# Kernel tuning notes

Hardware: AMD Instinct MI355X
Metric: run time of the kernel (lower is better)

The kernel has to match this reference:

```python
import jax, jax.numpy as jnp
import numpy as np

B, DIM, W0, H0 = 4, 256, 128, 128
HEADS, HEAD_DIM = 8, 32
FOLD, PROP = 2, 4
EPS_GN = 1e-5


def _l2norm(x):
    n = jnp.linalg.norm(x, axis=-1, keepdims=True)
    return x / jnp.maximum(n, 1e-12)  # matches F.normalize eps


def _fold(t, f):
    # (b, c, f*w, f*h) -> (b*f*f, c, w, h), matching einops '(b f1 f2)' ordering
    b, c, W, H = t.shape
    w, h = W // f, H // f
    return t.reshape(b, c, f, w, f, h).transpose(0, 2, 4, 1, 3, 5).reshape(b * f * f, c, w, h)


def _unfold(t, f, b0):
    bf, c, w, h = t.shape
    return t.reshape(b0, f, f, c, w, h).transpose(0, 3, 1, 4, 2, 5).reshape(b0, c, f * w, f * h)


def _pool(t, p):
    # AdaptiveAvgPool2d((p, p)) for divisible sizes
    b, c, w, h = t.shape
    return t.reshape(b, c, p, w // p, p, h // p).mean(axis=(3, 5))


def setup_inputs() -> dict:
    key = jax.random.key(0)
    ks = jax.random.split(key, 6)
    D = HEADS * HEAD_DIM
    return {
        "x": jax.random.normal(ks[0], (B, DIM, W0, H0), jnp.float32),
        "xyz": jax.random.normal(ks[1], (B, 3, W0, H0), jnp.float32),
        "Wv": jax.random.normal(ks[2], (D, DIM, 7, 7), jnp.float32) * 0.02,
        "bv": jnp.zeros((D,), jnp.float32),
        "Wproj": jax.random.normal(ks[3], (DIM, D), jnp.float32) * 0.02,
        "bproj": jnp.zeros((DIM,), jnp.float32),
        "gn_w": jnp.ones((D,), jnp.float32),
        "gn_b": jnp.zeros((D,), jnp.float32),
        "sim_alpha": jnp.ones((1,), jnp.float32),
        "sim_beta": jnp.zeros((1,), jnp.float32),
    }


def reference(x, xyz, Wv, bv, Wproj, bproj, gn_w, gn_b, sim_alpha, sim_beta):
    # value = self.v(x): 7x7 conv, padding 3
    value = jax.lax.conv_general_dilated(
        x, Wv, (1, 1), ((3, 3), (3, 3)),
        dimension_numbers=("NCHW", "OIHW", "NCHW")) + bv[None, :, None, None]
    b0 = x.shape[0]
    # heads split: 'b (e c) w h -> (b e) c w h'
    xh = x.reshape(b0 * HEADS, HEAD_DIM, W0, H0)
    vh = value.reshape(b0 * HEADS, HEAD_DIM, W0, H0)
    xf = _fold(xh, FOLD)
    vf = _fold(vh, FOLD)
    xyzf = _fold(xyz, FOLD)
    bb, c, w, h = xf.shape
    M = PROP * PROP
    N = w * h
    centers = _pool(xf, PROP)                                   # (bb, c, p, p)
    xyz_c = _pool(xyzf, PROP)
    value_centers = _pool(vf, PROP).reshape(bb, c, M).transpose(0, 2, 1)  # (bb, M, c)
    cen = centers.reshape(bb, c, M).transpose(0, 2, 1)          # (bb, M, c)
    xpts = xf.reshape(bb, c, N).transpose(0, 2, 1)              # (bb, N, c)
    vpts = vf.reshape(bb, c, N).transpose(0, 2, 1)              # (bb, N, c)
    sim = jax.nn.sigmoid(sim_beta + sim_alpha *
                         jnp.einsum('bmc,bnc->bmn', _l2norm(cen), _l2norm(xpts)))
    bg = xyzf.shape[0]
    xyz_pts = xyzf.reshape(bg, 3, N).transpose(0, 2, 1)
    xyz_cc = xyz_c.reshape(bg, 3, M).transpose(0, 2, 1)
    sim_geo = jax.nn.sigmoid(sim_beta + sim_alpha *
                             jnp.einsum('bmc,bnc->bmn', _l2norm(xyz_cc), _l2norm(xyz_pts)))
    sim_geo = jnp.tile(sim_geo, (sim.shape[0] // sim_geo.shape[0], 1, 1))  # torch .repeat
    sim = sim * sim_geo ** 2
    # faithful mask math: scatter_(1, argmax, 1.0) into an all-ones tensor leaves it all-ones,
    # so dense_mask == 1 and split_mask == 0 exactly as in the source.
    dense_mask = jnp.ones_like(sim)
    split_mask = 1.0 - dense_mask
    denss_sim = sim * dense_mask
    split_sim = sim * split_mask
    split_out = (jnp.einsum('bmn,bnc->bmc', split_sim, vpts) + value_centers) \
                / (split_sim.sum(-1, keepdims=True) + 1.0)
    denss_out = (jnp.einsum('bmn,bnc->bmc', denss_sim, xpts) + cen) \
                / (denss_sim.sum(-1, keepdims=True) + 1.0)
    denss_pts = jnp.einsum('bmc,bmn->bnc', denss_out, denss_sim)  # (bb, N, c)
    split_pts = jnp.einsum('bmc,bmn->bnc', split_out, split_sim)
    out = (denss_pts + split_pts).transpose(0, 2, 1).reshape(bb, c, w, h)
    out = _unfold(out, FOLD, b0 * HEADS)
    out = out.reshape(b0, HEADS * HEAD_DIM, W0, H0)
    # GroupNorm with 1 group: normalize over (C, H, W) per sample
    mu = out.mean(axis=(1, 2, 3), keepdims=True)
    var = ((out - mu) ** 2).mean(axis=(1, 2, 3), keepdims=True)
    out = (out - mu) / jnp.sqrt(var + EPS_GN)
    out = out * gn_w[None, :, None, None] + gn_b[None, :, None, None]
    # proj 1x1 conv + silu
    out = jnp.einsum('bchw,oc->bohw', out, Wproj) + bproj[None, :, None, None]
    return jax.nn.silu(out)
```

## Files before the change

### kernel.cpp

```cpp
#include <hip/hip_runtime.h>
#include <stdint.h>


typedef __attribute__((ext_vector_type(8))) short short8;
typedef __attribute__((ext_vector_type(4))) float floatx4;
typedef __fp16 fp16x2 __attribute__((ext_vector_type(2)));

#define SIMS_DW 260

__device__ float g_sbp[2048*2];
__device__ float g_alpha[1024];
__device__ float g_bias[1024];
__device__ __attribute__((aligned(16))) _Float16 g_Wa[4*256*256];
__device__ float g_cenraw[128*16*32];
__device__ float g_cenhat[128*16*32];
__device__ float g_gcenhat[16*16*4];
__device__ __attribute__((aligned(16))) _Float16 g_sim[(size_t)128*4096*16];
__device__ float g_dnum[128*16*16*32];
__device__ float g_rsum[128*16*16];
__device__ unsigned g_dnh2[128*256];
__device__ __attribute__((aligned(16))) _Float16 g_preout[(size_t)128*4096*32];

static __device__ __forceinline__ fp16x2 as_h2(unsigned u) { return __builtin_bit_cast(fp16x2, u); }
static __device__ __forceinline__ unsigned pk(float a, float b) {
  return __builtin_bit_cast(unsigned, __builtin_amdgcn_cvt_pkrtz(a, b));
}
#if __has_builtin(__builtin_amdgcn_fdot2)
static __device__ __forceinline__ float fdot2(fp16x2 a, fp16x2 b, float c) {
  return __builtin_amdgcn_fdot2(a, b, c, false);
}
#else
static __device__ __forceinline__ float fdot2(fp16x2 a, fp16x2 b, float c) {
  return c + (float)a[0]*(float)b[0] + (float)a[1]*(float)b[1];
}
#endif
static __device__ __forceinline__ float sum16(const float* p) {
  const float4* q = (const float4*)p;
  float4 a = q[0], b = q[1], c = q[2], d = q[3];
  return (a.x+a.y+a.z+a.w) + (b.x+b.y+b.z+b.w) + (c.x+c.y+c.z+c.w) + (d.x+d.y+d.z+d.w);
}
static __device__ __forceinline__ float sigm(float z) {
  return __builtin_amdgcn_rcpf(1.f + __expf(-z));
}

__global__ __launch_bounds__(64) void k0_geo(const float* __restrict__ xyz) {
  __shared__ float gc[64];
  const int gti = blockIdx.x;
  const int bg = gti >> 2, f1 = (gti >> 1) & 1, f2 = gti & 1;
  const int t = threadIdx.x;
  if (t < 48) {
    const int m = t / 3, ch = t - 3*(t/3);
    const int pi = m >> 2, pj = m & 3;
    const float* p = xyz + (size_t)(bg*3+ch)*16384 + (f1*64 + pi*16)*128 + f2*64 + pj*16;
    float s = 0.f;
    #pragma unroll
    for (int r = 0; r < 16; ++r) s += sum16(p + r*128);
    gc[m*4+ch] = s * (1.f/256.f);
  }
  __syncthreads();
  if (t < 16) {
    float g0 = gc[t*4], g1 = gc[t*4+1], g2 = gc[t*4+2];
    float inv = 1.f / fmaxf(sqrtf(g0*g0+g1*g1+g2*g2), 1e-12f);
    float* o = g_gcenhat + gti*64 + t*4;
    o[0] = g0*inv; o[1] = g1*inv; o[2] = g2*inv; o[3] = 0.f;
  }
}

__global__ __launch_bounds__(128) void k1a_cen(const float* __restrict__ x) {
  __shared__ float cenL[128];
  __shared__ float invL[4];
  const int blk = blockIdx.x;
  const int bb = blk >> 2, pi = blk & 3;
  const int b = bb >> 5, e = (bb >> 2) & 7, f1 = (bb >> 1) & 1, f2 = bb & 1;
  const int tid = threadIdx.x;
  const int c = tid >> 2, pj = tid & 3;
  const int m = pi*4 + pj;
  const float* p = x + ((size_t)(b*256 + e*32 + c)*128 + f1*64 + pi*16)*128 + f2*64 + pj*16;
  float s = 0.f;
  #pragma unroll
  for (int r = 0; r < 16; ++r) s += sum16(p + r*128);
  const float raw = s * (1.f/256.f);
  cenL[pj*32 + c] = raw;
  g_cenraw[(bb*16 + m)*32 + c] = raw;
  __syncthreads();
  if (tid < 4) {
    float ss = 0.f;
    #pragma unroll
    for (int cc = 0; cc < 32; ++cc) { float v = cenL[tid*32+cc]; ss += v*v; }
    invL[tid] = 1.f / fmaxf(sqrtf(ss), 1e-12f);
  }
  __syncthreads();
  g_cenhat[(bb*16 + m)*32 + c] = raw * invL[pj];
}

__global__ __launch_bounds__(256, 4) void k1b_sim(const float* __restrict__ x,
                                                  const float* __restrict__ xyz,
                                                  const float* __restrict__ salpha,
                                                  const float* __restrict__ sbeta) {
  __shared__ float simS[16*SIMS_DW];
  __shared__ unsigned chP[256];
  __shared__ float gcenL[64];
  __shared__ float rsW[64];
  const int blk = blockIdx.x;
  const int bb = blk >> 4, ck = blk & 15;
  const int b = bb >> 5, e = (bb >> 2) & 7, f1 = (bb >> 1) & 1, f2 = bb & 1;
  const int gti = ((e & 3) << 2) | (f1 << 1) | f2;
  const int tid = threadIdx.x, lane = tid & 63, wave = tid >> 6;
  const float alpha = salpha[0], beta = sbeta[0];
  const float* xt = x + (((size_t)(b*256 + e*32))*128 + f1*64)*128 + f2*64;

  {
    const float2 cp = *(const float2*)(g_cenhat + bb*512 + tid*2);
    chP[tid] = pk(cp.x, cp.y);
  }
  if (tid < 64) gcenL[tid] = g_gcenhat[gti*64 + tid];
  __syncthreads();

  const int ng = ck*256 + tid;
  const int wi = ng >> 6, hi = ng & 63;
  const int addr = wi*128 + hi;
  float xn[32]; float ss = 0.f;
  #pragma unroll
  for (int c = 0; c < 32; ++c) { float v = xt[(size_t)c*16384 + addr]; xn[c] = v; ss += v*v; }
  unsigned xp[16];
  #pragma unroll
  for (int p = 0; p < 16; ++p) xp[p] = pk(xn[2*p], xn[2*p+1]);
  const float invn = __builtin_amdgcn_rcpf(fmaxf(sqrtf(ss), 1e-12f));
  float g0, g1, g2;
  {
    const float* gp = xyz + (size_t)((e & 3)*3)*16384 + (f1*64 + wi)*128 + f2*64 + hi;
    g0 = gp[0]; g1 = gp[16384]; g2 = gp[32768];
    float invg = __builtin_amdgcn_rcpf(fmaxf(sqrtf(g0*g0+g1*g1+g2*g2), 1e-12f));
    g0 *= invg; g1 *= invg; g2 *= invg;
  }
  float svf[16];
  #pragma unroll
  for (int m = 0; m < 16; ++m) {
    float d = 0.f;
    #pragma unroll
    for (int p = 0; p < 16; ++p) d = fdot2(as_h2(chP[m*16+p]), as_h2(xp[p]), d);
    d *= invn;
    const float* gh = gcenL + m*4;
    const float dg = gh[0]*g0 + gh[1]*g1 + gh[2]*g2;
    const float s  = sigm(beta + alpha*d);
    const float gg = sigm(beta + alpha*dg);
    const float sv = s*gg*gg;
    svf[m] = sv;
    simS[m*SIMS_DW + tid] = sv;
  }
  {
    uint4 o0, o1;
    o0.x = pk(svf[0],svf[1]);   o0.y = pk(svf[2],svf[3]);
    o0.z = pk(svf[4],svf[5]);   o0.w = pk(svf[6],svf[7]);
    o1.x = pk(svf[8],svf[9]);   o1.y = pk(svf[10],svf[11]);
    o1.z = pk(svf[12],svf[13]); o1.w = pk(svf[14],svf[15]);
    _Float16* gp = g_sim + ((size_t)bb*4096 + ng)*16;
    *(uint4*)gp = o0;
    *(uint4*)(gp + 8) = o1;
  }
  #pragma unroll
  for (int m = 0; m < 16; ++m) {
    float v = svf[m];
    #pragma unroll
    for (int off = 1; off < 64; off <<= 1) v += __shfl_xor(v, off, 64);
    if (lane == 0) rsW[wave*16 + m] = v;
  }
  __syncthreads();
  if (tid < 16) g_rsum[(bb*16 + ck)*16 + tid] = rsW[tid] + rsW[16+tid] + rsW[32+tid] + rsW[48+tid];

  #pragma unroll
  for (int t2 = 0; t2 < 2; ++t2) {
    const int task = tid + t2*256;
    const int m = task & 15, c = task >> 4;
    const float* sp = simS + m*SIMS_DW;
    const float* px = xt + (size_t)c*16384 + ck*512;
    float acc = 0.f;
    #pragma unroll 2
    for (int j = 0; j < 32; ++j) {
      const int a0 = (j >> 3)*128 + (j & 7)*8;
      const float4 xa = *(const float4*)(px + a0);
      const float4 xb = *(const float4*)(px + a0 + 4);
      const float4 sa = *(const float4*)(sp + j*8);
      const float4 sb = *(const float4*)(sp + j*8 + 4);
      acc += sa.x*xa.x + sa.y*xa.y + sa.z*xa.z + sa.w*xa.w
           + sb.x*xb.x + sb.y*xb.y + sb.z*xb.z + sb.w*xb.w;
    }
    g_dnum[(((size_t)bb*16 + ck)*16 + m)*32 + c] = acc;
  }
}

__global__ __launch_bounds__(512) void k1c_red() {
  __shared__ float denssL[512];
  __shared__ float rsL[16];
  const int bb = blockIdx.x, tid = threadIdx.x;
  if (tid < 16) {
    float r = 1.f;
    #pragma unroll
    for (int k = 0; k < 16; ++k) r += g_rsum[(bb*16 + k)*16 + tid];
    rsL[tid] = r;
  }
  float a = g_cenraw[bb*512 + tid];
  #pragma unroll
  for (int k = 0; k < 16; ++k) a += g_dnum[(size_t)bb*8192 + k*512 + tid];
  __syncthreads();
  denssL[tid] = a / rsL[tid >> 5];
  __syncthreads();
  if (tid < 256) {
    const int c = tid >> 3, mp = tid & 7;
    g_dnh2[bb*256 + c*8 + mp] = pk(denssL[(2*mp)*32 + c], denssL[(2*mp+1)*32 + c]);
  }
}

__global__ __launch_bounds__(256, 4) void k1d_out() {
  __shared__ unsigned dl[256];
  __shared__ float sred[8];
  const int blk = blockIdx.x;
  const int bb = blk >> 4, ck = blk & 15;
  const int tid = threadIdx.x, lane = tid & 63, wave = tid >> 6;
  dl[tid] = g_dnh2[bb*256 + tid];
  __syncthreads();
  const int ng = ck*256 + tid;
  unsigned sp[8];
  {
    const _Float16* gp = g_sim + ((size_t)bb*4096 + ng)*16;
    const uint4 q0 = *(const uint4*)gp;
    const uint4 q1 = *(const uint4*)(gp + 8);
    sp[0]=q0.x; sp[1]=q0.y; sp[2]=q0.z; sp[3]=q0.w;
    sp[4]=q1.x; sp[5]=q1.y; sp[6]=q1.z; sp[7]=q1.w;
  }
  float out[32];
  #pragma unroll
  for (int c = 0; c < 32; ++c) {
    float acc = 0.f;
    #pragma unroll
    for (int mp = 0; mp < 8; ++mp) acc = fdot2(as_h2(sp[mp]), as_h2(dl[c*8 + mp]), acc);
    out[c] = acc;
  }
  float s1 = 0.f, s2 = 0.f;
  #pragma unroll
  for (int c = 0; c < 32; ++c) { s1 += out[c]; s2 += out[c]*out[c]; }
  {
    uint4 w[4];
    #pragma unroll
    for (int q = 0; q < 4; ++q) {
      w[q].x = pk(out[8*q+0], out[8*q+1]); w[q].y = pk(out[8*q+2], out[8*q+3]);
      w[q].z = pk(out[8*q+4], out[8*q+5]); w[q].w = pk(out[8*q+6], out[8*q+7]);
    }
    _Float16* gp = g_preout + ((size_t)bb*4096 + ng)*32;
    *(uint4*)gp = w[0]; *(uint4*)(gp+8) = w[1]; *(uint4*)(gp+16) = w[2]; *(uint4*)(gp+24) = w[3];
  }
  #pragma unroll
  for (int off = 1; off < 64; off <<= 1) { s1 += __shfl_xor(s1, off, 64); s2 += __shfl_xor(s2, off, 64); }
  if (lane == 0) { sred[wave] = s1; sred[4+wave] = s2; }
  __syncthreads();
  if (tid == 0) {
    g_sbp[blk*2]   = sred[0]+sred[1]+sred[2]+sred[3];
    g_sbp[blk*2+1] = sred[4]+sred[5]+sred[6]+sred[7];
  }
}

__global__ __launch_bounds__(256) void k2_prep(const float* __restrict__ Wp,
                                               const float* __restrict__ bpr,
                                               const float* __restrict__ gnw,
                                               const float* __restrict__ gnb) {
  __shared__ float betaL[256];
  __shared__ float alphaL[256];
  __shared__ float rr[8];
  const int b = blockIdx.x, t = threadIdx.x, lane = t & 63, wave = t >> 6;
  float s1 = g_sbp[(b*512 + t)*2]     + g_sbp[(b*512 + 256 + t)*2];
  float s2 = g_sbp[(b*512 + t)*2 + 1] + g_sbp[(b*512 + 256 + t)*2 + 1];
  #pragma unroll
  for (int off = 1; off < 64; off <<= 1) { s1 += __shfl_xor(s1, off, 64); s2 += __shfl_xor(s2, off, 64); }
  if (lane == 0) { rr[wave] = s1; rr[4+wave] = s2; }
  __syncthreads();
  const float S1 = rr[0]+rr[1]+rr[2]+rr[3];
  const float S2 = rr[4]+rr[5]+rr[6]+rr[7];
  const float inv_n = 1.f / 4194304.f;
  const float mu  = S1 * inv_n;
  const float inv = rsqrtf(fmaxf(S2*inv_n - mu*mu, 0.f) + 1e-5f);
  const float a = inv * gnw[t];
  g_alpha[b*256 + t] = a;
  alphaL[t] = a;
  betaL[t] = gnb[t] - mu * a;
  __syncthreads();
  float k = bpr[t];
  const float* wr = Wp + t*256;
  _Float16* wa = g_Wa + ((size_t)b*256 + t)*256;
  for (int c = 0; c < 256; c += 8) {
    const float4 w0 = *(const float4*)(wr + c);
    const float4 w1 = *(const float4*)(wr + c + 4);
    k += w0.x*betaL[c+0] + w0.y*betaL[c+1] + w0.z*betaL[c+2] + w0.w*betaL[c+3]
       + w1.x*betaL[c+4] + w1.y*betaL[c+5] + w1.z*betaL[c+6] + w1.w*betaL[c+7];
    uint4 o;
    o.x = pk(w0.x*alphaL[c+0], w0.y*alphaL[c+1]);
    o.y = pk(w0.z*alphaL[c+2], w0.w*alphaL[c+3]);
    o.z = pk(w1.x*alphaL[c+4], w1.y*alphaL[c+5]);
    o.w = pk(w1.z*alphaL[c+6], w1.w*alphaL[c+7]);
    *(uint4*)(wa + c) = o;
  }
  g_bias[b*256 + t] = k;
}

__global__ __launch_bounds__(256, 4) void k3_proj(float* __restrict__ out) {
  __shared__ float biasL[256];
  const int blk = blockIdx.x;
  const int b = blk >> 8, pb = blk & 255;
  const int f1 = pb >> 7, f2 = pb & 1;
  const int nbase = ((pb >> 1) & 63) * 64;
  const int tid = threadIdx.x, lane = tid & 63, wave = tid >> 6;
  const int lm = lane & 15, quad = lane >> 4;
  const int m0 = wave*64;
  biasL[tid] = g_bias[b*256 + tid];
  __syncthreads();
  floatx4 acc[4][4] = {};
  #pragma unroll
  for (int ks = 0; ks < 8; ++ks) {
    const _Float16* bbase = g_preout
        + ((size_t)(b*32 + ks*4 + f1*2 + f2)*4096 + nbase)*32 + quad*8;
    const _Float16* abase = g_Wa + ((size_t)b*256)*256 + (size_t)ks*32 + quad*8;
    short8 afr[4], bfr[4];
    #pragma unroll
    for (int mi = 0; mi < 4; ++mi)
      afr[mi] = *(const short8*)(abase + (size_t)(m0 + mi*16 + lm)*256);
    #pragma unroll
    for (int ni = 0; ni < 4; ++ni)
      bfr[ni] = *(const short8*)(bbase + (ni*16 + lm)*32);
    #pragma unroll
    for (int mi = 0; mi < 4; ++mi) {
      #pragma unroll
      for (int ni = 0; ni < 4; ++ni)
        acc[mi][ni] = __builtin_amdgcn_mfma_f32_16x16x32_f16(afr[mi], bfr[ni], acc[mi][ni], 0, 0, 0);
    }
  }
  #pragma unroll
  for (int mi = 0; mi < 4; ++mi) {
    #pragma unroll
    for (int r = 0; r < 4; ++r) {
      const int o = m0 + mi*16 + quad*4 + r;
      const float kb = biasL[o];
      #pragma unroll
      for (int ni = 0; ni < 4; ++ni) {
        float val = acc[mi][ni][r] + kb;
        val = val * sigm(val);
        out[((size_t)(b*256 + o))*16384 + pb*64 + ni*16 + lm] = val;
      }
    }
  }
}

extern "C" void kernel_launch(void* const* d_in, const int* in_sizes, int n_in,
                              void* d_out, int out_size, void* d_ws, size_t ws_size,
                              hipStream_t stream)
{
  (void)in_sizes; (void)n_in; (void)d_ws; (void)ws_size; (void)out_size;
  const float* x     = (const float*)d_in[0];
  const float* xyz   = (const float*)d_in[1];
  const float* Wproj = (const float*)d_in[4];
  const float* bproj = (const float*)d_in[5];
  const float* gnw   = (const float*)d_in[6];
  const float* gnb   = (const float*)d_in[7];
  const float* sa    = (const float*)d_in[8];
  const float* sb    = (const float*)d_in[9];
  float* out = (float*)d_out;

  hipLaunchKernelGGL(k0_geo,  dim3(16),   dim3(64),  0, stream, xyz);
  hipLaunchKernelGGL(k1a_cen, dim3(512),  dim3(128), 0, stream, x);
  hipLaunchKernelGGL(k1b_sim, dim3(2048), dim3(256), 0, stream, x, xyz, sa, sb);
  hipLaunchKernelGGL(k1c_red, dim3(128),  dim3(512), 0, stream);
  hipLaunchKernelGGL(k1d_out, dim3(2048), dim3(256), 0, stream);
  hipLaunchKernelGGL(k2_prep, dim3(4),    dim3(256), 0, stream, Wproj, bproj, gnw, gnb);
  hipLaunchKernelGGL(k3_proj, dim3(1024), dim3(256), 0, stream, out);
}
```

Before: 262.0 us.

## Fuse similarity, center reduction and output into one per-batch-head kernel

Merges k1b_sim, k1c_red and k1d_out into one kernel with one 1024-thread block per folded head. The full 4096x16 fp16 similarity matrix stays in LDS, so the global g_sim round trip, the partial dnum/rsum buffers and two launches go away. The sim^T·x reduction now runs on MFMA 16x16x32 f16 instead of scalar FMAs. The cost is only 128 blocks on a large GPU, a large LDS footprint limiting occupancy, and LDS atomics for the cross-wave reduction.

```diff
diff --git a/kernel.cpp b/kernel.cpp
--- a/kernel.cpp
+++ b/kernel.cpp
@@ -6,19 +6,12 @@
 typedef __attribute__((ext_vector_type(4))) float floatx4;
 typedef __fp16 fp16x2 __attribute__((ext_vector_type(2)));
 
-#define SIMS_DW 260
-
-__device__ float g_sbp[2048*2];
-__device__ float g_alpha[1024];
+__device__ float g_sbp[256];
 __device__ float g_bias[1024];
 __device__ __attribute__((aligned(16))) _Float16 g_Wa[4*256*256];
 __device__ float g_cenraw[128*16*32];
 __device__ float g_cenhat[128*16*32];
 __device__ float g_gcenhat[16*16*4];
-__device__ __attribute__((aligned(16))) _Float16 g_sim[(size_t)128*4096*16];
-__device__ float g_dnum[128*16*16*32];
-__device__ float g_rsum[128*16*16];
-__device__ unsigned g_dnh2[128*256];
 __device__ __attribute__((aligned(16))) _Float16 g_preout[(size_t)128*4096*32];
 
 static __device__ __forceinline__ fp16x2 as_h2(unsigned u) { return __builtin_bit_cast(fp16x2, u); }
@@ -93,169 +86,169 @@
   g_cenhat[(bb*16 + m)*32 + c] = raw * invL[pj];
 }
 
-__global__ __launch_bounds__(256, 4) void k1b_sim(const float* __restrict__ x,
-                                                  const float* __restrict__ xyz,
-                                                  const float* __restrict__ salpha,
-                                                  const float* __restrict__ sbeta) {
-  __shared__ float simS[16*SIMS_DW];
+__global__ __launch_bounds__(1024, 4) void kf_simout(const float* __restrict__ x,
+                                                     const float* __restrict__ xyz,
+                                                     const float* __restrict__ salpha,
+                                                     const float* __restrict__ sbeta) {
+  __shared__ __attribute__((aligned(16))) unsigned simL[4096*8];
   __shared__ unsigned chP[256];
+  __shared__ unsigned dl[256];
   __shared__ float gcenL[64];
-  __shared__ float rsW[64];
-  const int blk = blockIdx.x;
-  const int bb = blk >> 4, ck = blk & 15;
+  __shared__ float rsW[16*16];
+  __shared__ float dnumL[512];
+  __shared__ float sred[32];
+  const int bb = blockIdx.x;
   const int b = bb >> 5, e = (bb >> 2) & 7, f1 = (bb >> 1) & 1, f2 = bb & 1;
   const int gti = ((e & 3) << 2) | (f1 << 1) | f2;
   const int tid = threadIdx.x, lane = tid & 63, wave = tid >> 6;
+  const int lm = lane & 15, quad = lane >> 4;
   const float alpha = salpha[0], beta = sbeta[0];
   const float* xt = x + (((size_t)(b*256 + e*32))*128 + f1*64)*128 + f2*64;
-
-  {
+  const float* gxyz = xyz + (size_t)((e & 3)*3)*16384 + f1*8192 + f2*64;
+
+  if (tid < 256) {
     const float2 cp = *(const float2*)(g_cenhat + bb*512 + tid*2);
     chP[tid] = pk(cp.x, cp.y);
   }
   if (tid < 64) gcenL[tid] = g_gcenhat[gti*64 + tid];
-  __syncthreads();
-
-  const int ng = ck*256 + tid;
-  const int wi = ng >> 6, hi = ng & 63;
-  const int addr = wi*128 + hi;
-  float xn[32]; float ss = 0.f;
-  #pragma unroll
-  for (int c = 0; c < 32; ++c) { float v = xt[(size_t)c*16384 + addr]; xn[c] = v; ss += v*v; }
-  unsigned xp[16];
-  #pragma unroll
-  for (int p = 0; p < 16; ++p) xp[p] = pk(xn[2*p], xn[2*p+1]);
-  const float invn = __builtin_amdgcn_rcpf(fmaxf(sqrtf(ss), 1e-12f));
-  float g0, g1, g2;
-  {
-    const float* gp = xyz + (size_t)((e & 3)*3)*16384 + (f1*64 + wi)*128 + f2*64 + hi;
-    g0 = gp[0]; g1 = gp[16384]; g2 = gp[32768];
-    float invg = __builtin_amdgcn_rcpf(fmaxf(sqrtf(g0*g0+g1*g1+g2*g2), 1e-12f));
-    g0 *= invg; g1 *= invg; g2 *= invg;
-  }
-  float svf[16];
+  if (tid < 512) dnumL[tid] = 0.f;
+  __syncthreads();
+
+  float rs[16];
+  #pragma unroll
+  for (int m = 0; m < 16; ++m) rs[m] = 0.f;
+
+  #pragma unroll
+  for (int j = 0; j < 4; ++j) {
+    const int px = wave*256 + j*64 + lane;
+    const int addr = (wave*4 + j)*128 + lane;
+    float ss = 0.f;
+    unsigned xp[16];
+    #pragma unroll
+    for (int p = 0; p < 16; ++p) {
+      const float v0 = xt[(size_t)(2*p)*16384 + addr];
+      const float v1 = xt[(size_t)(2*p+1)*16384 + addr];
+      ss += v0*v0 + v1*v1;
+      xp[p] = pk(v0, v1);
+    }
+    const float invn = __builtin_amdgcn_rcpf(fmaxf(sqrtf(ss), 1e-12f));
+    float g0, g1, g2;
+    {
+      const float* gp = gxyz + addr;
+      g0 = gp[0]; g1 = gp[16384]; g2 = gp[32768];
+      const float invg = __builtin_amdgcn_rcpf(fmaxf(sqrtf(g0*g0+g1*g1+g2*g2), 1e-12f));
+      g0 *= invg; g1 *= invg; g2 *= invg;
+    }
+    unsigned sw[8];
+    #pragma unroll
+    for (int mp = 0; mp < 8; ++mp) {
+      const int m0 = 2*mp, m1 = 2*mp + 1;
+      float d0 = 0.f, d1 = 0.f;
+      #pragma unroll
+      for (int p = 0; p < 16; ++p) {
+        const fp16x2 xv = as_h2(xp[p]);
+        d0 = fdot2(as_h2(chP[m0*16 + p]), xv, d0);
+        d1 = fdot2(as_h2(chP[m1*16 + p]), xv, d1);
+      }
+      d0 *= invn; d1 *= invn;
+      const float* gh0 = gcenL + m0*4;
+      const float* gh1 = gcenL + m1*4;
+      const float dg0 = gh0[0]*g0 + gh0[1]*g1 + gh0[2]*g2;
+      const float dg1 = gh1[0]*g0 + gh1[1]*g1 + gh1[2]*g2;
+      const float s0  = sigm(beta + alpha*d0), gg0 = sigm(beta + alpha*dg0);
+      const float s1v = sigm(beta + alpha*d1), gg1 = sigm(beta + alpha*dg1);
+      const float sv0 = s0*gg0*gg0, sv1 = s1v*gg1*gg1;
+      rs[m0] += sv0; rs[m1] += sv1;
+      sw[mp] = pk(sv0, sv1);
+    }
+    *(uint4*)&simL[px*8]     = *(const uint4*)&sw[0];
+    *(uint4*)&simL[px*8 + 4] = *(const uint4*)&sw[4];
+  }
   #pragma unroll
   for (int m = 0; m < 16; ++m) {
-    float d = 0.f;
-    #pragma unroll
-    for (int p = 0; p < 16; ++p) d = fdot2(as_h2(chP[m*16+p]), as_h2(xp[p]), d);
-    d *= invn;
-    const float* gh = gcenL + m*4;
-    const float dg = gh[0]*g0 + gh[1]*g1 + gh[2]*g2;
-    const float s  = sigm(beta + alpha*d);
-    const float gg = sigm(beta + alpha*dg);
-    const float sv = s*gg*gg;
-    svf[m] = sv;
-    simS[m*SIMS_DW + tid] = sv;
-  }
-  {
-    uint4 o0, o1;
-    o0.x = pk(svf[0],svf[1]);   o0.y = pk(svf[2],svf[3]);
-    o0.z = pk(svf[4],svf[5]);   o0.w = pk(svf[6],svf[7]);
-    o1.x = pk(svf[8],svf[9]);   o1.y = pk(svf[10],svf[11]);
-    o1.z = pk(svf[12],svf[13]); o1.w = pk(svf[14],svf[15]);
-    _Float16* gp = g_sim + ((size_t)bb*4096 + ng)*16;
-    *(uint4*)gp = o0;
-    *(uint4*)(gp + 8) = o1;
-  }
-  #pragma unroll
-  for (int m = 0; m < 16; ++m) {
-    float v = svf[m];
+    float v = rs[m];
     #pragma unroll
     for (int off = 1; off < 64; off <<= 1) v += __shfl_xor(v, off, 64);
     if (lane == 0) rsW[wave*16 + m] = v;
   }
   __syncthreads();
-  if (tid < 16) g_rsum[(bb*16 + ck)*16 + tid] = rsW[tid] + rsW[16+tid] + rsW[32+tid] + rsW[48+tid];
-
-  #pragma unroll
-  for (int t2 = 0; t2 < 2; ++t2) {
-    const int task = tid + t2*256;
-    const int m = task & 15, c = task >> 4;
-    const float* sp = simS + m*SIMS_DW;
-    const float* px = xt + (size_t)c*16384 + ck*512;
-    float acc = 0.f;
-    #pragma unroll 2
-    for (int j = 0; j < 32; ++j) {
-      const int a0 = (j >> 3)*128 + (j & 7)*8;
-      const float4 xa = *(const float4*)(px + a0);
-      const float4 xb = *(const float4*)(px + a0 + 4);
-      const float4 sa = *(const float4*)(sp + j*8);
-      const float4 sb = *(const float4*)(sp + j*8 + 4);
-      acc += sa.x*xa.x + sa.y*xa.y + sa.z*xa.z + sa.w*xa.w
-           + sb.x*xb.x + sb.y*xb.y + sb.z*xb.z + sb.w*xb.w;
-    }
-    g_dnum[(((size_t)bb*16 + ck)*16 + m)*32 + c] = acc;
-  }
-}
-
-__global__ __launch_bounds__(512) void k1c_red() {
-  __shared__ float denssL[512];
-  __shared__ float rsL[16];
-  const int bb = blockIdx.x, tid = threadIdx.x;
-  if (tid < 16) {
-    float r = 1.f;
-    #pragma unroll
-    for (int k = 0; k < 16; ++k) r += g_rsum[(bb*16 + k)*16 + tid];
-    rsL[tid] = r;
-  }
-  float a = g_cenraw[bb*512 + tid];
-  #pragma unroll
-  for (int k = 0; k < 16; ++k) a += g_dnum[(size_t)bb*8192 + k*512 + tid];
-  __syncthreads();
-  denssL[tid] = a / rsL[tid >> 5];
-  __syncthreads();
+
+  {
+    floatx4 acc0 = {0.f,0.f,0.f,0.f}, acc1 = {0.f,0.f,0.f,0.f};
+    const _Float16* simH = (const _Float16*)simL;
+    #pragma unroll
+    for (int ks = 0; ks < 8; ++ks) {
+      const int kb = wave*256 + ks*32 + quad*8;
+      short8 af;
+      #pragma unroll
+      for (int t = 0; t < 8; ++t)
+        af[t] = __builtin_bit_cast(short, simH[(kb + t)*16 + lm]);
+      const int ag = ((kb >> 6)*128) + (kb & 63);
+      const float* pb0 = xt + (size_t)lm*16384 + ag;
+      const float* pb1 = pb0 + (size_t)16*16384;
+      short8 bf0, bf1;
+      #pragma unroll
+      for (int t = 0; t < 8; ++t) bf0[t] = __builtin_bit_cast(short, (_Float16)pb0[t]);
+      #pragma unroll
+      for (int t = 0; t < 8; ++t) bf1[t] = __builtin_bit_cast(short, (_Float16)pb1[t]);
+      acc0 = __builtin_amdgcn_mfma_f32_16x16x32_f16(af, bf0, acc0, 0, 0, 0);
+      acc1 = __builtin_amdgcn_mfma_f32_16x16x32_f16(af, bf1, acc1, 0, 0, 0);
+    }
+    #pragma unroll
+    for (int r = 0; r < 4; ++r) {
+      const int m = quad*4 + r;
+      atomicAdd(&dnumL[m*32 + lm],      acc0[r]);
+      atomicAdd(&dnumL[m*32 + 16 + lm], acc1[r]);
+    }
+  }
+  __syncthreads();
+
   if (tid < 256) {
     const int c = tid >> 3, mp = tid & 7;
-    g_dnh2[bb*256 + c*8 + mp] = pk(denssL[(2*mp)*32 + c], denssL[(2*mp+1)*32 + c]);
-  }
-}
-
-__global__ __launch_bounds__(256, 4) void k1d_out() {
-  __shared__ unsigned dl[256];
-  __shared__ float sred[8];
-  const int blk = blockIdx.x;
-  const int bb = blk >> 4, ck = blk & 15;
-  const int tid = threadIdx.x, lane = tid & 63, wave = tid >> 6;
-  dl[tid] = g_dnh2[bb*256 + tid];
-  __syncthreads();
-  const int ng = ck*256 + tid;
-  unsigned sp[8];
-  {
-    const _Float16* gp = g_sim + ((size_t)bb*4096 + ng)*16;
-    const uint4 q0 = *(const uint4*)gp;
-    const uint4 q1 = *(const uint4*)(gp + 8);
-    sp[0]=q0.x; sp[1]=q0.y; sp[2]=q0.z; sp[3]=q0.w;
-    sp[4]=q1.x; sp[5]=q1.y; sp[6]=q1.z; sp[7]=q1.w;
-  }
-  float out[32];
-  #pragma unroll
-  for (int c = 0; c < 32; ++c) {
-    float acc = 0.f;
-    #pragma unroll
-    for (int mp = 0; mp < 8; ++mp) acc = fdot2(as_h2(sp[mp]), as_h2(dl[c*8 + mp]), acc);
-    out[c] = acc;
-  }
+    const int m0 = 2*mp, m1 = 2*mp + 1;
+    float r0 = 1.f, r1 = 1.f;
+    #pragma unroll
+    for (int w = 0; w < 16; ++w) { r0 += rsW[w*16 + m0]; r1 += rsW[w*16 + m1]; }
+    const float d0 = (g_cenraw[bb*512 + m0*32 + c] + dnumL[m0*32 + c]) / r0;
+    const float d1 = (g_cenraw[bb*512 + m1*32 + c] + dnumL[m1*32 + c]) / r1;
+    dl[tid] = pk(d0, d1);
+  }
+  __syncthreads();
+
   float s1 = 0.f, s2 = 0.f;
   #pragma unroll
-  for (int c = 0; c < 32; ++c) { s1 += out[c]; s2 += out[c]*out[c]; }
-  {
-    uint4 w[4];
+  for (int j = 0; j < 4; ++j) {
+    const int px = wave*256 + j*64 + lane;
+    const uint4 q0 = *(const uint4*)&simL[px*8];
+    const uint4 q1 = *(const uint4*)&simL[px*8 + 4];
+    unsigned sp[8] = {q0.x, q0.y, q0.z, q0.w, q1.x, q1.y, q1.z, q1.w};
+    float out[32];
+    #pragma unroll
+    for (int c = 0; c < 32; ++c) {
+      float acc = 0.f;
+      #pragma unroll
+      for (int mp = 0; mp < 8; ++mp) acc = fdot2(as_h2(sp[mp]), as_h2(dl[c*8 + mp]), acc);
+      out[c] = acc; s1 += acc; s2 += acc*acc;
+    }
+    uint4 w4[4];
     #pragma unroll
     for (int q = 0; q < 4; ++q) {
-      w[q].x = pk(out[8*q+0], out[8*q+1]); w[q].y = pk(out[8*q+2], out[8*q+3]);
-      w[q].z = pk(out[8*q+4], out[8*q+5]); w[q].w = pk(out[8*q+6], out[8*q+7]);
-    }
-    _Float16* gp = g_preout + ((size_t)bb*4096 + ng)*32;
-    *(uint4*)gp = w[0]; *(uint4*)(gp+8) = w[1]; *(uint4*)(gp+16) = w[2]; *(uint4*)(gp+24) = w[3];
+      w4[q].x = pk(out[8*q+0], out[8*q+1]); w4[q].y = pk(out[8*q+2], out[8*q+3]);
+      w4[q].z = pk(out[8*q+4], out[8*q+5]); w4[q].w = pk(out[8*q+6], out[8*q+7]);
+    }
+    _Float16* gp = g_preout + ((size_t)bb*4096 + px)*32;
+    *(uint4*)gp = w4[0]; *(uint4*)(gp+8) = w4[1]; *(uint4*)(gp+16) = w4[2]; *(uint4*)(gp+24) = w4[3];
   }
   #pragma unroll
   for (int off = 1; off < 64; off <<= 1) { s1 += __shfl_xor(s1, off, 64); s2 += __shfl_xor(s2, off, 64); }
-  if (lane == 0) { sred[wave] = s1; sred[4+wave] = s2; }
+  if (lane == 0) { sred[wave] = s1; sred[16 + wave] = s2; }
   __syncthreads();
   if (tid == 0) {
-    g_sbp[blk*2]   = sred[0]+sred[1]+sred[2]+sred[3];
-    g_sbp[blk*2+1] = sred[4]+sred[5]+sred[6]+sred[7];
+    float a = 0.f, q = 0.f;
+    #pragma unroll
+    for (int w = 0; w < 16; ++w) { a += sred[w]; q += sred[16 + w]; }
+    g_sbp[bb*2]     = a;
+    g_sbp[bb*2 + 1] = q;
   }
 }
 
@@ -265,21 +258,22 @@
                                                const float* __restrict__ gnb) {
   __shared__ float betaL[256];
   __shared__ float alphaL[256];
-  __shared__ float rr[8];
-  const int b = blockIdx.x, t = threadIdx.x, lane = t & 63, wave = t >> 6;
-  float s1 = g_sbp[(b*512 + t)*2]     + g_sbp[(b*512 + 256 + t)*2];
-  float s2 = g_sbp[(b*512 + t)*2 + 1] + g_sbp[(b*512 + 256 + t)*2 + 1];
-  #pragma unroll
-  for (int off = 1; off < 64; off <<= 1) { s1 += __shfl_xor(s1, off, 64); s2 += __shfl_xor(s2, off, 64); }
-  if (lane == 0) { rr[wave] = s1; rr[4+wave] = s2; }
-  __syncthreads();
-  const float S1 = rr[0]+rr[1]+rr[2]+rr[3];
-  const float S2 = rr[4]+rr[5]+rr[6]+rr[7];
+  __shared__ float S12[2];
+  const int b = blockIdx.x, t = threadIdx.x;
+  if (t < 64) {
+    float v1 = 0.f, v2 = 0.f;
+    if (t < 32) { v1 = g_sbp[(b*32 + t)*2]; v2 = g_sbp[(b*32 + t)*2 + 1]; }
+    #pragma unroll
+    for (int off = 1; off < 64; off <<= 1) { v1 += __shfl_xor(v1, off, 64); v2 += __shfl_xor(v2, off, 64); }
+    if (t == 0) { S12[0] = v1; S12[1] = v2; }
+  }
+  __syncthreads();
+  const float S1 = S12[0];
+  const float S2 = S12[1];
   const float inv_n = 1.f / 4194304.f;
   const float mu  = S1 * inv_n;
   const float inv = rsqrtf(fmaxf(S2*inv_n - mu*mu, 0.f) + 1e-5f);
   const float a = inv * gnw[t];
-  g_alpha[b*256 + t] = a;
   alphaL[t] = a;
   betaL[t] = gnb[t] - mu * a;
   __syncthreads();
@@ -363,11 +357,9 @@
   const float* sb    = (const float*)d_in[9];
   float* out = (float*)d_out;
 
-  hipLaunchKernelGGL(k0_geo,  dim3(16),   dim3(64),  0, stream, xyz);
-  hipLaunchKernelGGL(k1a_cen, dim3(512),  dim3(128), 0, stream, x);
-  hipLaunchKernelGGL(k1b_sim, dim3(2048), dim3(256), 0, stream, x, xyz, sa, sb);
-  hipLaunchKernelGGL(k1c_red, dim3(128),  dim3(512), 0, stream);
-  hipLaunchKernelGGL(k1d_out, dim3(2048), dim3(256), 0, stream);
-  hipLaunchKernelGGL(k2_prep, dim3(4),    dim3(256), 0, stream, Wproj, bproj, gnw, gnb);
-  hipLaunchKernelGGL(k3_proj, dim3(1024), dim3(256), 0, stream, out);
-}
+  hipLaunchKernelGGL(k0_geo,    dim3(16),   dim3(64),   0, stream, xyz);
+  hipLaunchKernelGGL(k1a_cen,   dim3(512),  dim3(128),  0, stream, x);
+  hipLaunchKernelGGL(kf_simout, dim3(128),  dim3(1024), 0, stream, x, xyz, sa, sb);
+  hipLaunchKernelGGL(k2_prep,   dim3(4),    dim3(256),  0, stream, Wproj, bproj, gnw, gnb);
+  hipLaunchKernelGGL(k3_proj,   dim3(1024), dim3(256),  0, stream, out);
+}
```

Result: slower. 750.1 us (+186.3%).

## Use MFMA for similarity dot products and partial numerator reduction in k1b_sim

Applied to the files above, without the earlier changes.

Rewrites the k1b_sim kernel so the 16x32 center-by-pixel cosine dot products are computed with 16x16x32 fp16 MFMA instead of per-thread fdot2 loops. The sim-weighted x reduction (dnum) also moves to MFMA, with per-wave results combined through LDS atomics. Similarity values are now staged in LDS as fp16 with a padded row stride, and the xyz gating term is precomputed into a separate LDS table. This offloads scalar FMA work to the matrix cores at the cost of more LDS traffic, extra barriers, fp16 rounding of the x operand in the dnum product, and shared-memory atomics.

```diff
diff --git a/kernel.cpp b/kernel.cpp
--- a/kernel.cpp
+++ b/kernel.cpp
@@ -6,7 +6,7 @@
 typedef __attribute__((ext_vector_type(4))) float floatx4;
 typedef __fp16 fp16x2 __attribute__((ext_vector_type(2)));
 
-#define SIMS_DW 260
+#define SIMW 264
 
 __device__ float g_sbp[2048*2];
 __device__ float g_alpha[1024];
@@ -97,15 +97,19 @@
                                                   const float* __restrict__ xyz,
                                                   const float* __restrict__ salpha,
                                                   const float* __restrict__ sbeta) {
-  __shared__ float simS[16*SIMS_DW];
-  __shared__ unsigned chP[256];
+  __shared__ __attribute__((aligned(16))) unsigned  xL[256*20];
+  __shared__ __attribute__((aligned(16))) _Float16 simS[16*SIMW];
+  __shared__ __attribute__((aligned(16))) _Float16 gT[16*SIMW];
+  __shared__ __attribute__((aligned(16))) unsigned chP[16*16];
   __shared__ float gcenL[64];
-  __shared__ float rsW[64];
+  __shared__ float rsW[4*16];
+  __shared__ float dnumL[512];
   const int blk = blockIdx.x;
   const int bb = blk >> 4, ck = blk & 15;
   const int b = bb >> 5, e = (bb >> 2) & 7, f1 = (bb >> 1) & 1, f2 = bb & 1;
   const int gti = ((e & 3) << 2) | (f1 << 1) | f2;
   const int tid = threadIdx.x, lane = tid & 63, wave = tid >> 6;
+  const int lm = lane & 15, quad = lane >> 4;
   const float alpha = salpha[0], beta = sbeta[0];
   const float* xt = x + (((size_t)(b*256 + e*32))*128 + f1*64)*128 + f2*64;
 
@@ -114,79 +118,116 @@
     chP[tid] = pk(cp.x, cp.y);
   }
   if (tid < 64) gcenL[tid] = g_gcenhat[gti*64 + tid];
+  dnumL[tid] = 0.f; dnumL[tid + 256] = 0.f;
   __syncthreads();
 
   const int ng = ck*256 + tid;
   const int wi = ng >> 6, hi = ng & 63;
   const int addr = wi*128 + hi;
-  float xn[32]; float ss = 0.f;
-  #pragma unroll
-  for (int c = 0; c < 32; ++c) { float v = xt[(size_t)c*16384 + addr]; xn[c] = v; ss += v*v; }
-  unsigned xp[16];
-  #pragma unroll
-  for (int p = 0; p < 16; ++p) xp[p] = pk(xn[2*p], xn[2*p+1]);
-  const float invn = __builtin_amdgcn_rcpf(fmaxf(sqrtf(ss), 1e-12f));
-  float g0, g1, g2;
+  {
+    float ss = 0.f;
+    unsigned xp[16];
+    #pragma unroll
+    for (int p = 0; p < 16; ++p) {
+      const float v0 = xt[(size_t)(2*p)*16384 + addr];
+      const float v1 = xt[(size_t)(2*p+1)*16384 + addr];
+      ss += v0*v0 + v1*v1;
+      xp[p] = pk(v0, v1);
+    }
+    uint4 u0 = {xp[0],xp[1],xp[2],xp[3]};
+    uint4 u1 = {xp[4],xp[5],xp[6],xp[7]};
+    uint4 u2 = {xp[8],xp[9],xp[10],xp[11]};
+    uint4 u3 = {xp[12],xp[13],xp[14],xp[15]};
+    *(uint4*)(xL + tid*20)      = u0;
+    *(uint4*)(xL + tid*20 + 4)  = u1;
+    *(uint4*)(xL + tid*20 + 8)  = u2;
+    *(uint4*)(xL + tid*20 + 12) = u3;
+    const float invn = __builtin_amdgcn_rcpf(fmaxf(sqrtf(ss), 1e-12f));
+    ((float*)xL)[tid*20 + 16] = invn;
+  }
   {
     const float* gp = xyz + (size_t)((e & 3)*3)*16384 + (f1*64 + wi)*128 + f2*64 + hi;
-    g0 = gp[0]; g1 = gp[16384]; g2 = gp[32768];
-    float invg = __builtin_amdgcn_rcpf(fmaxf(sqrtf(g0*g0+g1*g1+g2*g2), 1e-12f));
+    float g0 = gp[0], g1 = gp[16384], g2 = gp[32768];
+    const float invg = __builtin_amdgcn_rcpf(fmaxf(sqrtf(g0*g0+g1*g1+g2*g2), 1e-12f));
     g0 *= invg; g1 *= invg; g2 *= invg;
-  }
-  float svf[16];
-  #pragma unroll
-  for (int m = 0; m < 16; ++m) {
-    float d = 0.f;
-    #pragma unroll
-    for (int p = 0; p < 16; ++p) d = fdot2(as_h2(chP[m*16+p]), as_h2(xp[p]), d);
-    d *= invn;
-    const float* gh = gcenL + m*4;
-    const float dg = gh[0]*g0 + gh[1]*g1 + gh[2]*g2;
-    const float s  = sigm(beta + alpha*d);
-    const float gg = sigm(beta + alpha*dg);
-    const float sv = s*gg*gg;
-    svf[m] = sv;
-    simS[m*SIMS_DW + tid] = sv;
-  }
-  {
-    uint4 o0, o1;
-    o0.x = pk(svf[0],svf[1]);   o0.y = pk(svf[2],svf[3]);
-    o0.z = pk(svf[4],svf[5]);   o0.w = pk(svf[6],svf[7]);
-    o1.x = pk(svf[8],svf[9]);   o1.y = pk(svf[10],svf[11]);
-    o1.z = pk(svf[12],svf[13]); o1.w = pk(svf[14],svf[15]);
+    #pragma unroll
+    for (int m = 0; m < 16; ++m) {
+      const float* gh = gcenL + m*4;
+      const float dg = gh[0]*g0 + gh[1]*g1 + gh[2]*g2;
+      const float gg = sigm(beta + alpha*dg);
+      gT[m*SIMW + tid] = (_Float16)(gg*gg);
+    }
+  }
+  __syncthreads();
+
+  {
+    const short8 afx = *(const short8*)((const _Float16*)chP + lm*32 + quad*8);
+    float rsacc[4] = {0.f, 0.f, 0.f, 0.f};
+    #pragma unroll
+    for (int t = 0; t < 4; ++t) {
+      const int px = wave*64 + t*16 + lm;
+      const short8 bfx = *(const short8*)((const _Float16*)xL + px*40 + quad*8);
+      floatx4 d = {0.f,0.f,0.f,0.f};
+      d = __builtin_amdgcn_mfma_f32_16x16x32_f16(afx, bfx, d, 0, 0, 0);
+      const float invn = ((const float*)xL)[px*20 + 16];
+      #pragma unroll
+      for (int r = 0; r < 4; ++r) {
+        const int m = quad*4 + r;
+        const float gg2 = (float)gT[m*SIMW + px];
+        const float sv = sigm(beta + alpha * d[r] * invn) * gg2;
+        rsacc[r] += sv;
+        simS[m*SIMW + px] = (_Float16)sv;
+      }
+    }
+    #pragma unroll
+    for (int r = 0; r < 4; ++r) {
+      float v = rsacc[r];
+      v += __shfl_xor(v, 1, 64); v += __shfl_xor(v, 2, 64);
+      v += __shfl_xor(v, 4, 64); v += __shfl_xor(v, 8, 64);
+      if (lm == 0) rsW[wave*16 + quad*4 + r] = v;
+    }
+  }
+  __syncthreads();
+
+  {
+    unsigned w[8];
+    const unsigned short* sp = (const unsigned short*)simS;
+    #pragma unroll
+    for (int p = 0; p < 8; ++p)
+      w[p] = (unsigned)sp[(2*p)*SIMW + tid] | ((unsigned)sp[(2*p+1)*SIMW + tid] << 16);
     _Float16* gp = g_sim + ((size_t)bb*4096 + ng)*16;
-    *(uint4*)gp = o0;
-    *(uint4*)(gp + 8) = o1;
-  }
-  #pragma unroll
-  for (int m = 0; m < 16; ++m) {
-    float v = svf[m];
-    #pragma unroll
-    for (int off = 1; off < 64; off <<= 1) v += __shfl_xor(v, off, 64);
-    if (lane == 0) rsW[wave*16 + m] = v;
-  }
-  __syncthreads();
-  if (tid < 16) g_rsum[(bb*16 + ck)*16 + tid] = rsW[tid] + rsW[16+tid] + rsW[32+tid] + rsW[48+tid];
-
-  #pragma unroll
-  for (int t2 = 0; t2 < 2; ++t2) {
-    const int task = tid + t2*256;
-    const int m = task & 15, c = task >> 4;
-    const float* sp = simS + m*SIMS_DW;
-    const float* px = xt + (size_t)c*16384 + ck*512;
-    float acc = 0.f;
-    #pragma unroll 2
-    for (int j = 0; j < 32; ++j) {
-      const int a0 = (j >> 3)*128 + (j & 7)*8;
-      const float4 xa = *(const float4*)(px + a0);
-      const float4 xb = *(const float4*)(px + a0 + 4);
-      const float4 sa = *(const float4*)(sp + j*8);
-      const float4 sb = *(const float4*)(sp + j*8 + 4);
-      acc += sa.x*xa.x + sa.y*xa.y + sa.z*xa.z + sa.w*xa.w
-           + sb.x*xb.x + sb.y*xb.y + sb.z*xb.z + sb.w*xb.w;
-    }
-    g_dnum[(((size_t)bb*16 + ck)*16 + m)*32 + c] = acc;
-  }
+    *(uint4*)gp       = *(const uint4*)&w[0];
+    *(uint4*)(gp + 8) = *(const uint4*)&w[4];
+  }
+  if (tid < 16)
+    g_rsum[(bb*16 + ck)*16 + tid] = rsW[tid] + rsW[16+tid] + rsW[32+tid] + rsW[48+tid];
+
+  {
+    floatx4 acc0 = {0.f,0.f,0.f,0.f}, acc1 = {0.f,0.f,0.f,0.f};
+    #pragma unroll
+    for (int ks = 0; ks < 2; ++ks) {
+      const int kb = wave*64 + ks*32 + quad*8;
+      const short8 af = *(const short8*)(simS + lm*SIMW + kb);
+      const int ag = ck*512 + ((kb >> 6)*128) + (kb & 63);
+      const float* pb0 = xt + (size_t)lm*16384 + ag;
+      const float* pb1 = pb0 + (size_t)16*16384;
+      short8 bf0, bf1;
+      #pragma unroll
+      for (int t = 0; t < 8; ++t) bf0[t] = __builtin_bit_cast(short, (_Float16)pb0[t]);
+      #pragma unroll
+      for (int t = 0; t < 8; ++t) bf1[t] = __builtin_bit_cast(short, (_Float16)pb1[t]);
+      acc0 = __builtin_amdgcn_mfma_f32_16x16x32_f16(af, bf0, acc0, 0, 0, 0);
+      acc1 = __builtin_amdgcn_mfma_f32_16x16x32_f16(af, bf1, acc1, 0, 0, 0);
+    }
+    #pragma unroll
+    for (int r = 0; r < 4; ++r) {
+      atomicAdd(&dnumL[(quad*4 + r)*32 + lm],      acc0[r]);
+      atomicAdd(&dnumL[(quad*4 + r)*32 + 16 + lm], acc1[r]);
+    }
+  }
+  __syncthreads();
+  g_dnum[(size_t)(bb*16 + ck)*512 + tid]       = dnumL[tid];
+  g_dnum[(size_t)(bb*16 + ck)*512 + 256 + tid] = dnumL[tid + 256];
 }
 
 __global__ __launch_bounds__(512) void k1c_red() {
```

Measured after the change: 250.9 us. 4.2% less time.
